# Optimization experiments

Hardware: AMD Instinct MI355X
Metric: run time of the kernel (lower is better)

Reference implementation:

```python
import jax, jax.numpy as jnp
import numpy as np

B, D, L, E, H = 8192, 1024, 256, 16, 400

def setup_inputs() -> dict:
    key = jax.random.key(0)
    ks = jax.random.split(key, 6)
    s1 = 1.0 / np.sqrt(D)
    s2 = 1.0 / np.sqrt(H)
    return {
        "x": jax.random.normal(ks[0], (B, D), dtype=jnp.float32),
        "angle_idx": jax.random.randint(ks[1], (B,), 0, E, dtype=jnp.int64),
        "W1": jax.random.uniform(ks[2], (E, D, H), jnp.float32, -s1, s1),
        "b1": jax.random.uniform(ks[3], (E, H), jnp.float32, -s1, s1),
        "W2": jax.random.uniform(ks[4], (E, H, 2 * L), jnp.float32, -s2, s2),
        "b2": jax.random.uniform(ks[5], (E, 2 * L), jnp.float32, -s2, s2),
    }

def reference(x, angle_idx, W1, b1, W2, b2):
    # Dense all-experts compute, then per-sample select (jit-friendly MoE dispatch).
    # h1: [E, B, H]
    h1 = jax.nn.relu(jnp.einsum('bd,edh->ebh', x, W1) + b1[:, None, :])
    # h: [E, B, 2L]
    h = jnp.einsum('ebh,ehk->ebk', h1, W2) + b2[:, None, :]
    sel = h[angle_idx, jnp.arange(x.shape[0])]  # [B, 2L], each row from its routed expert
    half = sel.shape[1] // 2
    z_mu, z_logvar = sel[:, :half], sel[:, half:]
    return (z_mu, z_logvar)
```

## Files before the change

kernel.cpp:

```cpp
#include <hip/hip_runtime.h>
#include <hip/hip_bf16.h>
#include <cstdint>
#include <cstddef>

#define B_N 8192
#define D_K 1024
#define H_N 400
#define HP  416
#define K2_N 512
#define E_N 16
#define L_N 256
#define TM 64
#define PAD_ROWS (B_N + E_N * TM)
#define NTILES (PAD_ROWS / TM)

typedef short bf16x8 __attribute__((ext_vector_type(8)));
typedef float f32x4 __attribute__((ext_vector_type(4)));

#define GLDS(gp, lp) __builtin_amdgcn_global_load_lds( \
    (const __attribute__((address_space(1))) unsigned int*)(gp), \
    (__attribute__((address_space(3))) unsigned int*)(lp), 16, 0, 0)

static __device__ __forceinline__ unsigned short f2bf(float f) {
  union { float f; unsigned int u; } c; c.f = f;
  unsigned int u = c.u + 0x7fffu + ((c.u >> 16) & 1u);
  return (unsigned short)(u >> 16);
}
static __device__ __forceinline__ unsigned int pkbf(float a, float b) {
  union { __hip_bfloat162 v; unsigned int u; } c;
  c.v = __float22bfloat162_rn(make_float2(a, b));
  return c.u;
}

__global__ __launch_bounds__(256) void hist_kernel(const int* __restrict__ idx,
                                                   int* __restrict__ hist) {
  __shared__ int h[E_N];
  const int t = threadIdx.x;
  if (t < E_N) h[t] = 0;
  __syncthreads();
  atomicAdd(&h[idx[blockIdx.x * 256 + t]], 1);
  __syncthreads();
  if (t < E_N) hist[blockIdx.x * E_N + t] = h[t];
}

__global__ __launch_bounds__(256) void prep_kernel(const float* __restrict__ W1,
                                                   const float* __restrict__ W2,
                                                   const float* __restrict__ x,
                                                   const int* __restrict__ idx,
                                                   const int* __restrict__ hist,
                                                   unsigned short* __restrict__ Wt1,
                                                   unsigned short* __restrict__ Wt2,
                                                   unsigned short* __restrict__ xc,
                                                   int* __restrict__ off_al,
                                                   int* __restrict__ cnt_al,
                                                   int* __restrict__ order) {
  const int bid = blockIdx.x;
  const int t = threadIdx.x;
  if (bid < 2688) {
    __shared__ unsigned short Ls[64][72];
    const float* S; unsigned short* Dt; int K, N, Kd, Nd, k0, n0;
    if (bid < 1792) {
      int e = bid / 112, r = bid % 112;
      k0 = (r % 16) * 64; n0 = (r / 16) * 64;
      S = W1 + (size_t)e * D_K * H_N; Dt = Wt1 + (size_t)e * HP * D_K;
      K = D_K; N = H_N; Kd = D_K; Nd = HP;
    } else {
      int t2 = bid - 1792; int e = t2 / 56, r = t2 % 56;
      k0 = (r % 7) * 64; n0 = (r / 7) * 64;
      S = W2 + (size_t)e * H_N * K2_N; Dt = Wt2 + (size_t)e * K2_N * HP;
      K = H_N; N = K2_N; Kd = HP; Nd = K2_N;
    }
    const int kk = t >> 4;
    const int nn = (t & 15) * 4;
    float4 v[4];
#pragma unroll
    for (int p = 0; p < 4; ++p) {
      int k = k0 + p * 16 + kk;
      int n = n0 + nn;
      v[p] = make_float4(0.f, 0.f, 0.f, 0.f);
      if (k < K && n + 3 < N) v[p] = *(const float4*)(S + (size_t)k * N + n);
    }
#pragma unroll
    for (int p = 0; p < 4; ++p) {
      Ls[nn + 0][p * 16 + kk] = f2bf(v[p].x);
      Ls[nn + 1][p * 16 + kk] = f2bf(v[p].y);
      Ls[nn + 2][p * 16 + kk] = f2bf(v[p].z);
      Ls[nn + 3][p * 16 + kk] = f2bf(v[p].w);
    }
    __syncthreads();
    const int n2 = t >> 3;
    const int ch = t & 7;
#pragma unroll
    for (int p = 0; p < 2; ++p) {
      int n = n0 + p * 32 + n2;
      int k = k0 + ch * 8;
      if (n < Nd && k < Kd)
        *(uint4*)(Dt + (size_t)n * Kd + k) = *(const uint4*)&Ls[p * 32 + n2][ch * 8];
    }
  } else if (bid < 3200) {
    const int xb = bid - 2688;
    const float* S = x + (size_t)xb * 16 * D_K;
    unsigned short* Dp = xc + (size_t)xb * 16 * D_K;
#pragma unroll
    for (int i = 0; i < 16; ++i) {
      float4 v = *(const float4*)(S + i * D_K + t * 4);
      uint2 o; o.x = pkbf(v.x, v.y); o.y = pkbf(v.z, v.w);
      *(uint2*)(Dp + i * D_K + t * 4) = o;
    }
  } else {
    const int hb = bid - 3200;
    __shared__ int totL[E_N], preL[E_N], offsL[E_N], curL[E_N];
    if (t < E_N) {
      int pre = 0, tot = 0;
      for (int b = 0; b < 32; ++b) {
        int h = hist[b * E_N + t];
        if (b < hb) pre += h;
        tot += h;
      }
      totL[t] = tot; preL[t] = pre;
    }
    __syncthreads();
    if (t == 0) {
      int acc = 0;
      for (int e = 0; e < E_N; ++e) {
        offsL[e] = acc;
        if (hb == 0) off_al[e] = acc;
        acc += ((totL[e] + TM - 1) / TM) * TM;
      }
      if (hb == 0) off_al[E_N] = acc;
    }
    __syncthreads();
    if (t < E_N) {
      curL[t] = offsL[t] + preL[t];
      if (hb == 0) cnt_al[t] = totL[t];
    }
    __syncthreads();
    const int b = hb * 256 + t;
    const int e = idx[b];
    const int slot = atomicAdd(&curL[e], 1);
    order[slot] = b;
    if (hb == 0) *(uint2*)(xc + (size_t)B_N * D_K + t * 4) = make_uint2(0, 0);
  }
}

__global__ __launch_bounds__(256) void gemm1_kernel(const unsigned short* __restrict__ xc,
                                                    const unsigned short* __restrict__ Wt1,
                                                    const float* __restrict__ b1,
                                                    const int* __restrict__ off_al,
                                                    const int* __restrict__ cnt_al,
                                                    const int* __restrict__ order,
                                                    unsigned short* __restrict__ h1buf) {
  __shared__ unsigned short As[2][64 * 32];
  __shared__ unsigned short Bs[2][64 * 32];
  __shared__ int offs[E_N + 1];
  __shared__ int rowidx[TM];
  const int tid = threadIdx.x;
  const int m0 = blockIdx.x * TM;
  const int nb = blockIdx.y;
  const int tstart = (nb < 5) ? 4 * nb : 20 + 3 * (nb - 5);
  const int tcnt   = (nb < 5) ? 4 : 3;
  if (tid <= E_N) offs[tid] = off_al[tid];
  __syncthreads();
  if (m0 >= offs[E_N]) return;
  int e = 0;
  while (m0 >= offs[e + 1]) ++e;
  if (tid < TM) {
    const bool valid = (m0 + tid) < (offs[e] + cnt_al[e]);
    rowidx[tid] = valid ? order[m0 + tid] : B_N;
  }
  __syncthreads();
  const unsigned short* Wt1e = Wt1 + (size_t)e * HP * D_K;

  const int l = tid & 63, w = tid >> 6;
  const int r4 = l >> 2;
  const int sg = (r4 ^ (r4 >> 2)) & 3;
  const int g8 = ((l & 3) ^ sg) * 8;
  const bool wact = (w < tcnt);
  const unsigned short* gA = xc + (size_t)rowidx[16 * w + r4] * D_K + g8;
  const unsigned short* gB = Wt1e + (size_t)((tstart + w) * 16 + r4) * D_K + g8;

  const int ln = l & 15, q = l >> 4;
  const int sr = (ln ^ (ln >> 2)) & 3;
  const int cq = (q ^ sr) * 8;

  f32x4 acc[4] = {};

  GLDS(gA, &As[0][16 * w * 32]);
  if (wact) GLDS(gB, &Bs[0][16 * w * 32]);

  for (int k0 = 0; k0 < D_K; k0 += 32) {
    const int cur = (k0 >> 5) & 1;
    const int nxt = cur ^ 1;
    __syncthreads();
    if (k0 + 32 < D_K) {
      GLDS(gA + k0 + 32, &As[nxt][16 * w * 32]);
      if (wact) GLDS(gB + k0 + 32, &Bs[nxt][16 * w * 32]);
    }
    if (wact) {
      bf16x8 af[4];
#pragma unroll
      for (int i = 0; i < 4; ++i)
        af[i] = *(const bf16x8*)&As[cur][(16 * i + ln) * 32 + cq];
      bf16x8 bfr = *(const bf16x8*)&Bs[cur][(16 * w + ln) * 32 + cq];
#pragma unroll
      for (int i = 0; i < 4; ++i)
        acc[i] = __builtin_amdgcn_mfma_f32_16x16x32_bf16(af[i], bfr, acc[i], 0, 0, 0);
    }
  }

  if (wact) {
    const int n = (tstart + w) * 16 + ln;
    if (n < H_N) {
      const float bias = b1[e * H_N + n];
#pragma unroll
      for (int i = 0; i < 4; ++i)
#pragma unroll
        for (int r = 0; r < 4; ++r) {
          const int m = m0 + 16 * i + 4 * q + r;
          h1buf[(size_t)m * HP + n] = f2bf(fmaxf(acc[i][r] + bias, 0.f));
        }
    }
  }
}

__global__ __launch_bounds__(256) void gemm2_kernel(const unsigned short* __restrict__ h1buf,
                                                    const unsigned short* __restrict__ Wt2,
                                                    const float* __restrict__ b2,
                                                    const int* __restrict__ off_al,
                                                    const int* __restrict__ cnt_al,
                                                    const int* __restrict__ order,
                                                    float* __restrict__ out) {
  __shared__ unsigned short As[2][64 * 32];
  __shared__ unsigned short Bs[2][64 * 32];
  __shared__ int offs[E_N + 1];
  __shared__ int rowidx[TM];
  const int tid = threadIdx.x;
  const int m0 = blockIdx.x * TM;
  const int nb = blockIdx.y;
  if (tid <= E_N) offs[tid] = off_al[tid];
  __syncthreads();
  if (m0 >= offs[E_N]) return;
  int e = 0;
  while (m0 >= offs[e + 1]) ++e;
  if (tid < TM) {
    const bool valid = (m0 + tid) < (offs[e] + cnt_al[e]);
    rowidx[tid] = valid ? order[m0 + tid] : -1;
  }
  __syncthreads();
  const unsigned short* Wt2e = Wt2 + (size_t)e * K2_N * HP;

  const int l = tid & 63, w = tid >> 6;
  const int r4 = l >> 2;
  const int sg = (r4 ^ (r4 >> 2)) & 3;
  const int g8 = ((l & 3) ^ sg) * 8;
  const unsigned short* gA = h1buf + (size_t)(m0 + 16 * w + r4) * HP + g8;
  const unsigned short* gB = Wt2e + (size_t)((4 * nb + w) * 16 + r4) * HP + g8;

  const int ln = l & 15, q = l >> 4;
  const int sr = (ln ^ (ln >> 2)) & 3;
  const int cq = (q ^ sr) * 8;

  f32x4 acc[4] = {};

  GLDS(gA, &As[0][16 * w * 32]);
  GLDS(gB, &Bs[0][16 * w * 32]);

  for (int k0 = 0; k0 < HP; k0 += 32) {
    const int cur = (k0 >> 5) & 1;
    const int nxt = cur ^ 1;
    __syncthreads();
    if (k0 + 32 < HP) {
      GLDS(gA + k0 + 32, &As[nxt][16 * w * 32]);
      GLDS(gB + k0 + 32, &Bs[nxt][16 * w * 32]);
    }
    bf16x8 af[4];
#pragma unroll
    for (int i = 0; i < 4; ++i)
      af[i] = *(const bf16x8*)&As[cur][(16 * i + ln) * 32 + cq];
    bf16x8 bfr = *(const bf16x8*)&Bs[cur][(16 * w + ln) * 32 + cq];
#pragma unroll
    for (int i = 0; i < 4; ++i)
      acc[i] = __builtin_amdgcn_mfma_f32_16x16x32_bf16(af[i], bfr, acc[i], 0, 0, 0);
  }

  const int n = (4 * nb + w) * 16 + ln;
  const float bias = b2[e * K2_N + n];
#pragma unroll
  for (int i = 0; i < 4; ++i)
#pragma unroll
    for (int r = 0; r < 4; ++r) {
      const int s = rowidx[16 * i + 4 * q + r];
      if (s >= 0) {
        const float v = acc[i][r] + bias;
        if (n < L_N) out[(size_t)s * L_N + n] = v;
        else         out[(size_t)(B_N + s) * L_N + (n - L_N)] = v;
      }
    }
}

extern "C" void kernel_launch(void* const* d_in, const int* in_sizes, int n_in,
                              void* d_out, int out_size, void* d_ws, size_t ws_size,
                              hipStream_t stream) {
  const float* x   = (const float*)d_in[0];
  const int*   idx = (const int*)d_in[1];
  const float* W1  = (const float*)d_in[2];
  const float* b1  = (const float*)d_in[3];
  const float* W2  = (const float*)d_in[4];
  const float* b2  = (const float*)d_in[5];
  float* out = (float*)d_out;

  char* ws = (char*)d_ws;
  int* off_al = (int*)(ws + 0);
  int* cnt_al = (int*)(ws + 128);
  int* hist   = (int*)(ws + 192);
  int* order  = (int*)(ws + 2240);
  unsigned short* xc  = (unsigned short*)(ws + 39104);
  unsigned short* h1  = (unsigned short*)(ws + 16818368);
  unsigned short* Wt1 = (unsigned short*)(ws + 24486080);
  unsigned short* Wt2 = (unsigned short*)(ws + 38117568);

  hist_kernel<<<32, 256, 0, stream>>>(idx, hist);
  prep_kernel<<<3232, 256, 0, stream>>>(W1, W2, x, idx, hist, Wt1, Wt2, xc,
                                        off_al, cnt_al, order);
  gemm1_kernel<<<dim3(NTILES, 7), 256, 0, stream>>>(xc, Wt1, b1, off_al, cnt_al, order, h1);
  gemm2_kernel<<<dim3(NTILES, 8), 256, 0, stream>>>(h1, Wt2, b2, off_al, cnt_al, order, out);
}
```

Before: 160.6 us.

## Fold histogram into prep kernel and remap GEMM grids for XCD locality

Removes the separate histogram kernel launch. Each routing block in the prep kernel now recomputes the per-expert totals and prefix counts itself, using wave ballots over the whole index array. The GEMM grids are flattened to 1D and remapped so that each XCD (round-robin by block id & 7) handles a contiguous range of 18 M-tiles across all N-blocks. The goal is to improve L2 reuse of the expert weights and the A tiles. In exchange, the 32 routing blocks each redundantly scan all 8192 indices with 16 ballots per element group.

Measured after the change: 165.1 us. +2.9%, slower.

```diff
diff --git a/kernel.cpp b/kernel.cpp
--- a/kernel.cpp
+++ b/kernel.cpp
@@ -32,22 +32,10 @@
   return c.u;
 }
 
-__global__ __launch_bounds__(256) void hist_kernel(const int* __restrict__ idx,
-                                                   int* __restrict__ hist) {
-  __shared__ int h[E_N];
-  const int t = threadIdx.x;
-  if (t < E_N) h[t] = 0;
-  __syncthreads();
-  atomicAdd(&h[idx[blockIdx.x * 256 + t]], 1);
-  __syncthreads();
-  if (t < E_N) hist[blockIdx.x * E_N + t] = h[t];
-}
-
 __global__ __launch_bounds__(256) void prep_kernel(const float* __restrict__ W1,
                                                    const float* __restrict__ W2,
                                                    const float* __restrict__ x,
                                                    const int* __restrict__ idx,
-                                                   const int* __restrict__ hist,
                                                    unsigned short* __restrict__ Wt1,
                                                    unsigned short* __restrict__ Wt2,
                                                    unsigned short* __restrict__ xc,
@@ -109,15 +97,27 @@
     }
   } else {
     const int hb = bid - 3200;
+    const int w = t >> 6, lane = t & 63;
+    __shared__ int totW[4][E_N], preW[4][E_N];
     __shared__ int totL[E_N], preL[E_N], offsL[E_N], curL[E_N];
+    int tot = 0, pre = 0;
+    for (int r = 0; r < 32; ++r) {
+      int v = idx[r * 256 + w * 64 + lane];
+#pragma unroll
+      for (int e = 0; e < E_N; ++e) {
+        unsigned long long m = __ballot(v == e);
+        if (lane == e) {
+          int c = __popcll(m);
+          tot += c;
+          if (r < hb) pre += c;
+        }
+      }
+    }
+    if (lane < E_N) { totW[w][lane] = tot; preW[w][lane] = pre; }
+    __syncthreads();
     if (t < E_N) {
-      int pre = 0, tot = 0;
-      for (int b = 0; b < 32; ++b) {
-        int h = hist[b * E_N + t];
-        if (b < hb) pre += h;
-        tot += h;
-      }
-      totL[t] = tot; preL[t] = pre;
+      totL[t] = totW[0][t] + totW[1][t] + totW[2][t] + totW[3][t];
+      preL[t] = preW[0][t] + preW[1][t] + preW[2][t] + preW[3][t];
     }
     __syncthreads();
     if (t == 0) {
@@ -155,8 +155,12 @@
   __shared__ int offs[E_N + 1];
   __shared__ int rowidx[TM];
   const int tid = threadIdx.x;
-  const int m0 = blockIdx.x * TM;
-  const int nb = blockIdx.y;
+  const int id = blockIdx.x;
+  const int xcd = id & 7;
+  const int rest = id >> 3;
+  const int nb = rest % 7;
+  const int mtile = xcd * 18 + rest / 7;
+  const int m0 = mtile * TM;
   const int tstart = (nb < 5) ? 4 * nb : 20 + 3 * (nb - 5);
   const int tcnt   = (nb < 5) ? 4 : 3;
   if (tid <= E_N) offs[tid] = off_al[tid];
@@ -235,8 +239,12 @@
   __shared__ int offs[E_N + 1];
   __shared__ int rowidx[TM];
   const int tid = threadIdx.x;
-  const int m0 = blockIdx.x * TM;
-  const int nb = blockIdx.y;
+  const int id = blockIdx.x;
+  const int xcd = id & 7;
+  const int rest = id >> 3;
+  const int nb = rest & 7;
+  const int mtile = xcd * 18 + (rest >> 3);
+  const int m0 = mtile * TM;
   if (tid <= E_N) offs[tid] = off_al[tid];
   __syncthreads();
   if (m0 >= offs[E_N]) return;
@@ -312,16 +320,14 @@
   char* ws = (char*)d_ws;
   int* off_al = (int*)(ws + 0);
   int* cnt_al = (int*)(ws + 128);
-  int* hist   = (int*)(ws + 192);
   int* order  = (int*)(ws + 2240);
   unsigned short* xc  = (unsigned short*)(ws + 39104);
   unsigned short* h1  = (unsigned short*)(ws + 16818368);
   unsigned short* Wt1 = (unsigned short*)(ws + 24486080);
   unsigned short* Wt2 = (unsigned short*)(ws + 38117568);
 
-  hist_kernel<<<32, 256, 0, stream>>>(idx, hist);
-  prep_kernel<<<3232, 256, 0, stream>>>(W1, W2, x, idx, hist, Wt1, Wt2, xc,
+  prep_kernel<<<3232, 256, 0, stream>>>(W1, W2, x, idx, Wt1, Wt2, xc,
                                         off_al, cnt_al, order);
-  gemm1_kernel<<<dim3(NTILES, 7), 256, 0, stream>>>(xc, Wt1, b1, off_al, cnt_al, order, h1);
-  gemm2_kernel<<<dim3(NTILES, 8), 256, 0, stream>>>(h1, Wt2, b2, off_al, cnt_al, order, out);
-}
+  gemm1_kernel<<<1008, 256, 0, stream>>>(xc, Wt1, b1, off_al, cnt_al, order, h1);
+  gemm2_kernel<<<1152, 256, 0, stream>>>(h1, Wt2, b2, off_al, cnt_al, order, out);
+}
```
